# Kernel tuning notes

Measured on AMD Instinct MI355X. Metric: run time of the kernel, lower is better.

Reference implementation:

```python
import jax, jax.numpy as jnp
import numpy as np

TEMPERATURE = 0.1

def setup_inputs() -> dict:
    key = jax.random.key(0)
    ks = jax.random.split(key, 6)
    B, K, D, H, N = 256, 32, 128, 256, 16
    z = jax.random.normal(ks[0], (B, K, D), dtype=jnp.float32)
    # edge MLP params: Linear(2D->H), GELU, Linear(H->D)
    W1 = jax.random.normal(ks[1], (2 * D, H), dtype=jnp.float32) * (1.0 / np.sqrt(2 * D))
    b1 = jnp.zeros((H,), dtype=jnp.float32)
    W2 = jax.random.normal(ks[2], (H, D), dtype=jnp.float32) * (1.0 / np.sqrt(H))
    b2 = jnp.zeros((D,), dtype=jnp.float32)
    codebook = jax.random.normal(ks[3], (N, D), dtype=jnp.float32) * 0.02
    return {"z": z, "W1": W1, "b1": b1, "W2": W2, "b2": b2, "codebook": codebook}

def reference(z, W1, b1, W2, b2, codebook):
    # z: (B,K,D). Edge MLP on concat([z_i, z_j]) == split-weight GEMMs,
    # avoiding materializing the (B,K,K,2D) concat tensor.
    D = z.shape[-1]
    h_i = jnp.einsum('bkd,dh->bkh', z, W1[:D])   # contribution of z_i
    h_j = jnp.einsum('bkd,dh->bkh', z, W1[D:])   # contribution of z_j
    h = h_i[:, :, None, :] + h_j[:, None, :, :] + b1       # (B,K,K,H)
    h = jax.nn.gelu(h, approximate=False)                    # torch nn.GELU default = exact erf
    e_ij = jnp.einsum('bijh,hd->bijd', h, W2) + b2           # (B,K,K,D)
    logits = jnp.einsum('bijd,nd->bijn', e_ij, codebook) / TEMPERATURE  # (B,K,K,N)
    alpha_ij = jax.nn.softmax(logits, axis=-1)
    m_ij = jnp.einsum('bijn,nd->bijd', alpha_ij, codebook)   # (B,K,K,D)
    return (m_ij, alpha_ij, e_ij, logits)
```

## Files before the change

kernel.cpp:

```cpp
#include <hip/hip_runtime.h>
#include <hip/hip_bf16.h>
#include <math.h>

#define BB 256
#define KK 32
#define DD 128
#define HH 256
#define NN 16
#define O0 ((size_t)0)
#define O1 ((size_t)33554432)
#define O2 ((size_t)37748736)
#define O3 ((size_t)71303168)

typedef float f32x4 __attribute__((ext_vector_type(4)));
typedef short s16x8 __attribute__((ext_vector_type(8)));

static __device__ __forceinline__ short f2bf(float x) {
  __hip_bfloat16 h = __float2bfloat16(x);
  return *reinterpret_cast<short*>(&h);
}
static __device__ __forceinline__ float bf2f(short s) {
  __hip_bfloat16 h;
  *reinterpret_cast<short*>(&h) = s;
  return __bfloat162float(h);
}

static __device__ __forceinline__ float gelu_exact(float x) {
  float ax = fabsf(x) * 0.70710678118654752f;
  float t = __builtin_amdgcn_rcpf(fmaf(0.3275911f, ax, 1.0f));
  float p = fmaf(1.061405429f, t, -1.453152027f);
  p = fmaf(p, t, 1.421413741f);
  p = fmaf(p, t, -0.284496736f);
  p = fmaf(p, t, 0.254829592f);
  p *= t;
  float e = __expf(-ax * ax);
  float er = fmaf(-p, e, 1.0f);
  er = copysignf(er, x);
  return 0.5f * x * (1.0f + er);
}

__global__ __launch_bounds__(256) void prep_kernel(
    const float* __restrict__ z, const float* __restrict__ W1,
    const float* __restrict__ W2, const float* __restrict__ cb,
    short* __restrict__ zb, short* __restrict__ W1th, short* __restrict__ W1tl,
    short* __restrict__ Wh, short* __restrict__ Wl,
    short* __restrict__ cbh, short* __restrict__ cbl) {
  const int idx = blockIdx.x * 256 + threadIdx.x;
  zb[idx] = f2bf(z[idx]);
  if (idx < 512 * 128) {
    int c = idx >> 7, k = idx & 127;
    float w = (c < 256) ? W1[(size_t)k * 256 + c]
                        : W1[(size_t)(128 + k) * 256 + (c - 256)];
    short h = f2bf(w);
    W1th[idx] = h;
    W1tl[idx] = f2bf(w - bf2f(h));
  }
  if (idx < 128 * 256) {
    int c = idx >> 8, k = idx & 255;
    float w = W2[(size_t)k * 128 + c];
    short h = f2bf(w);
    Wh[idx] = h;
    Wl[idx] = f2bf(w - bf2f(h));
  }
  if (idx < 2048) {
    float v = cb[idx];
    short h = f2bf(v);
    cbh[idx] = h;
    cbl[idx] = f2bf(v - bf2f(h));
  }
}

__global__ __launch_bounds__(256) void hproj_mfma(
    const short* __restrict__ zb, const short* __restrict__ W1th,
    const short* __restrict__ W1tl, float* __restrict__ H) {
  const int tid = threadIdx.x;
  const int lane = tid & 63;
  const int wv = tid >> 6;
  const int l4 = lane >> 4, l15 = lane & 15;
  const int row0 = blockIdx.x * 32;
  const int col0 = blockIdx.y * 128 + wv * 32;

  f32x4 acc[2][2];
#pragma unroll
  for (int mt = 0; mt < 2; ++mt)
#pragma unroll
    for (int nt = 0; nt < 2; ++nt)
      acc[mt][nt] = (f32x4){0.f, 0.f, 0.f, 0.f};

#pragma unroll
  for (int ks = 0; ks < 4; ++ks) {
    const int kof = ks * 32 + l4 * 8;
    s16x8 a0 = *(const s16x8*)(zb + (size_t)(row0 + l15) * 128 + kof);
    s16x8 a1 = *(const s16x8*)(zb + (size_t)(row0 + 16 + l15) * 128 + kof);
    s16x8 bh0 = *(const s16x8*)(W1th + (size_t)(col0 + l15) * 128 + kof);
    s16x8 bh1 = *(const s16x8*)(W1th + (size_t)(col0 + 16 + l15) * 128 + kof);
    s16x8 bl0 = *(const s16x8*)(W1tl + (size_t)(col0 + l15) * 128 + kof);
    s16x8 bl1 = *(const s16x8*)(W1tl + (size_t)(col0 + 16 + l15) * 128 + kof);
    acc[0][0] = __builtin_amdgcn_mfma_f32_16x16x32_bf16(a0, bh0, acc[0][0], 0, 0, 0);
    acc[0][0] = __builtin_amdgcn_mfma_f32_16x16x32_bf16(a0, bl0, acc[0][0], 0, 0, 0);
    acc[0][1] = __builtin_amdgcn_mfma_f32_16x16x32_bf16(a0, bh1, acc[0][1], 0, 0, 0);
    acc[0][1] = __builtin_amdgcn_mfma_f32_16x16x32_bf16(a0, bl1, acc[0][1], 0, 0, 0);
    acc[1][0] = __builtin_amdgcn_mfma_f32_16x16x32_bf16(a1, bh0, acc[1][0], 0, 0, 0);
    acc[1][0] = __builtin_amdgcn_mfma_f32_16x16x32_bf16(a1, bl0, acc[1][0], 0, 0, 0);
    acc[1][1] = __builtin_amdgcn_mfma_f32_16x16x32_bf16(a1, bh1, acc[1][1], 0, 0, 0);
    acc[1][1] = __builtin_amdgcn_mfma_f32_16x16x32_bf16(a1, bl1, acc[1][1], 0, 0, 0);
  }

#pragma unroll
  for (int mt = 0; mt < 2; ++mt)
#pragma unroll
    for (int nt = 0; nt < 2; ++nt)
#pragma unroll
      for (int r = 0; r < 4; ++r)
        H[(size_t)(row0 + mt * 16 + l4 * 4 + r) * 512 + col0 + nt * 16 + l15] =
            acc[mt][nt][r];
}

__global__ __launch_bounds__(256, 4) void pair_kernel(
    const float* __restrict__ Hcat, const float* __restrict__ b1,
    const short* __restrict__ Wh, const short* __restrict__ Wl,
    const float* __restrict__ b2, const float* __restrict__ cb,
    const short* __restrict__ cbh, const short* __restrict__ cbl,
    float* __restrict__ out) {
  __shared__ short sAh[32 * 256];
  __shared__ union {
    short Al[32 * 256];
    struct { short Eh[32 * 128]; short El[32 * 128]; } e;
  } u;
  __shared__ float sAlp[32][16];

  const int tid = threadIdx.x;
  const int blk = blockIdx.x;
  const int b = blk >> 5;

  {
    const int k0 = (tid & 127) * 2;
    const int pb = (tid >> 7) * 16;
    const float2 hiv = *(const float2*)(Hcat + (size_t)blk * 512 + k0);
    const float2 b1v = *(const float2*)(b1 + k0);
    const float hx = hiv.x + b1v.x;
    const float hy = hiv.y + b1v.y;
    const float* hjp = Hcat + ((size_t)b * KK + pb) * 512 + 256 + k0;
    unsigned* aH = (unsigned*)sAh;
    unsigned* aL = (unsigned*)u.Al;
    const int cw = tid & 127;
#pragma unroll 4
    for (int p = 0; p < 16; ++p) {
      const int row = pb + p;
      float2 hj = *(const float2*)(hjp + (size_t)p * 512);
      float g0 = gelu_exact(hx + hj.x);
      float g1 = gelu_exact(hy + hj.y);
      short h0 = f2bf(g0), h1 = f2bf(g1);
      short l0 = f2bf(g0 - bf2f(h0)), l1 = f2bf(g1 - bf2f(h1));
      const int wi = row * 128 + ((cw ^ ((row & 7) << 2)));
      aH[wi] = (unsigned)(unsigned short)h0 | ((unsigned)(unsigned short)h1 << 16);
      aL[wi] = (unsigned)(unsigned short)l0 | ((unsigned)(unsigned short)l1 << 16);
    }
  }
  __syncthreads();

  const int lane = tid & 63;
  const int wv = tid >> 6;
  const int nb = wv * 32;
  const int l4 = lane >> 4;
  const int l15 = lane & 15;

  f32x4 acc[2][2];
#pragma unroll
  for (int mt = 0; mt < 2; ++mt)
#pragma unroll
    for (int nt = 0; nt < 2; ++nt)
      acc[mt][nt] = (f32x4){0.f, 0.f, 0.f, 0.f};

  const int sw = (l15 & 7) << 4;
  const char* pAh = (const char*)sAh;
  const char* pAl = (const char*)u.Al;
  const size_t gB0 = (size_t)(nb + l15) * 256 + l4 * 8;

#pragma unroll
  for (int ks = 0; ks < 8; ++ks) {
    const int cbyte = ks * 64 + l4 * 16;
    const int o0 = l15 * 512 + (cbyte ^ sw);
    const int o1 = (16 + l15) * 512 + (cbyte ^ sw);
    s16x8 ah0 = *(const s16x8*)(pAh + o0);
    s16x8 ah1 = *(const s16x8*)(pAh + o1);
    s16x8 al0 = *(const s16x8*)(pAl + o0);
    s16x8 al1 = *(const s16x8*)(pAl + o1);
    const size_t g0 = gB0 + ks * 32;
    const size_t g1 = g0 + 16 * 256;
    s16x8 bh0 = *(const s16x8*)(Wh + g0);
    s16x8 bh1 = *(const s16x8*)(Wh + g1);
    s16x8 bl0 = *(const s16x8*)(Wl + g0);
    s16x8 bl1 = *(const s16x8*)(Wl + g1);

    acc[0][0] = __builtin_amdgcn_mfma_f32_16x16x32_bf16(ah0, bh0, acc[0][0], 0, 0, 0);
    acc[0][0] = __builtin_amdgcn_mfma_f32_16x16x32_bf16(al0, bh0, acc[0][0], 0, 0, 0);
    acc[0][0] = __builtin_amdgcn_mfma_f32_16x16x32_bf16(ah0, bl0, acc[0][0], 0, 0, 0);
    acc[0][1] = __builtin_amdgcn_mfma_f32_16x16x32_bf16(ah0, bh1, acc[0][1], 0, 0, 0);
    acc[0][1] = __builtin_amdgcn_mfma_f32_16x16x32_bf16(al0, bh1, acc[0][1], 0, 0, 0);
    acc[0][1] = __builtin_amdgcn_mfma_f32_16x16x32_bf16(ah0, bl1, acc[0][1], 0, 0, 0);
    acc[1][0] = __builtin_amdgcn_mfma_f32_16x16x32_bf16(ah1, bh0, acc[1][0], 0, 0, 0);
    acc[1][0] = __builtin_amdgcn_mfma_f32_16x16x32_bf16(al1, bh0, acc[1][0], 0, 0, 0);
    acc[1][0] = __builtin_amdgcn_mfma_f32_16x16x32_bf16(ah1, bl0, acc[1][0], 0, 0, 0);
    acc[1][1] = __builtin_amdgcn_mfma_f32_16x16x32_bf16(ah1, bh1, acc[1][1], 0, 0, 0);
    acc[1][1] = __builtin_amdgcn_mfma_f32_16x16x32_bf16(al1, bh1, acc[1][1], 0, 0, 0);
    acc[1][1] = __builtin_amdgcn_mfma_f32_16x16x32_bf16(ah1, bl1, acc[1][1], 0, 0, 0);
  }

  __syncthreads();

  {
    const float b2v0 = b2[nb + l15];
    const float b2v1 = b2[nb + 16 + l15];
    float* eg = out + O2 + (size_t)blk * (KK * DD);
    char* pEh = (char*)u.e.Eh;
    char* pEl = (char*)u.e.El;
#pragma unroll
    for (int mt = 0; mt < 2; ++mt) {
#pragma unroll
      for (int r = 0; r < 4; ++r) {
        const int row = mt * 16 + l4 * 4 + r;
        const int rsw = (row & 7) << 4;
        const float e0 = acc[mt][0][r] + b2v0;
        const float e1 = acc[mt][1][r] + b2v1;
        eg[row * 128 + nb + l15] = e0;
        eg[row * 128 + nb + 16 + l15] = e1;
        short h0 = f2bf(e0), h1 = f2bf(e1);
        short lo0 = f2bf(e0 - bf2f(h0)), lo1 = f2bf(e1 - bf2f(h1));
        const int i0 = row * 256 + (((nb + l15) * 2) ^ rsw);
        const int i1 = row * 256 + (((nb + 16 + l15) * 2) ^ rsw);
        *(short*)(pEh + i0) = h0;
        *(short*)(pEh + i1) = h1;
        *(short*)(pEl + i0) = lo0;
        *(short*)(pEl + i1) = lo1;
      }
    }
  }
  __syncthreads();

  if (wv < 2) {
    const int mrow = wv * 16;
    f32x4 lacc = (f32x4){0.f, 0.f, 0.f, 0.f};
    const char* pEh = (const char*)u.e.Eh;
    const char* pEl = (const char*)u.e.El;
    const int rowa = mrow + l15;
    const int rsw = (rowa & 7) << 4;
#pragma unroll
    for (int ks = 0; ks < 4; ++ks) {
      const int cbyte = ks * 64 + l4 * 16;
      const int o = rowa * 256 + (cbyte ^ rsw);
      s16x8 eh = *(const s16x8*)(pEh + o);
      s16x8 el = *(const s16x8*)(pEl + o);
      const size_t g = (size_t)l15 * 128 + ks * 32 + l4 * 8;
      s16x8 ch = *(const s16x8*)(cbh + g);
      s16x8 cl = *(const s16x8*)(cbl + g);
      lacc = __builtin_amdgcn_mfma_f32_16x16x32_bf16(eh, ch, lacc, 0, 0, 0);
      lacc = __builtin_amdgcn_mfma_f32_16x16x32_bf16(el, ch, lacc, 0, 0, 0);
      lacc = __builtin_amdgcn_mfma_f32_16x16x32_bf16(eh, cl, lacc, 0, 0, 0);
    }
    float* lg_out = out + O3 + (size_t)blk * (KK * NN);
    float* ag_out = out + O1 + (size_t)blk * (KK * NN);
#pragma unroll
    for (int r = 0; r < 4; ++r) {
      const int row = mrow + l4 * 4 + r;
      float lg = lacc[r] * 10.0f;
      float mx = lg;
#pragma unroll
      for (int m = 1; m < 16; m <<= 1) mx = fmaxf(mx, __shfl_xor(mx, m));
      float p = __expf(lg - mx);
      float s = p;
#pragma unroll
      for (int m = 1; m < 16; m <<= 1) s += __shfl_xor(s, m);
      float a = p / s;
      lg_out[row * 16 + l15] = lg;
      ag_out[row * 16 + l15] = a;
      sAlp[row][l15] = a;
    }
  }
  __syncthreads();

  {
    const int pg = tid >> 5;
    const int cg = tid & 31;
    const float4* cb4 = (const float4*)cb;
    float4 mac0 = make_float4(0.f, 0.f, 0.f, 0.f);
    float4 mac1 = mac0, mac2 = mac0, mac3 = mac0;
#pragma unroll
    for (int n = 0; n < 16; ++n) {
      float4 cv = cb4[n * 32 + cg];
      float a0 = sAlp[pg * 4 + 0][n];
      float a1 = sAlp[pg * 4 + 1][n];
      float a2 = sAlp[pg * 4 + 2][n];
      float a3 = sAlp[pg * 4 + 3][n];
      mac0.x += a0 * cv.x; mac0.y += a0 * cv.y; mac0.z += a0 * cv.z; mac0.w += a0 * cv.w;
      mac1.x += a1 * cv.x; mac1.y += a1 * cv.y; mac1.z += a1 * cv.z; mac1.w += a1 * cv.w;
      mac2.x += a2 * cv.x; mac2.y += a2 * cv.y; mac2.z += a2 * cv.z; mac2.w += a2 * cv.w;
      mac3.x += a3 * cv.x; mac3.y += a3 * cv.y; mac3.z += a3 * cv.z; mac3.w += a3 * cv.w;
    }
    float* mg = out + O0 + (size_t)blk * (KK * DD);
    *(float4*)(mg + (size_t)(pg * 4 + 0) * 128 + cg * 4) = mac0;
    *(float4*)(mg + (size_t)(pg * 4 + 1) * 128 + cg * 4) = mac1;
    *(float4*)(mg + (size_t)(pg * 4 + 2) * 128 + cg * 4) = mac2;
    *(float4*)(mg + (size_t)(pg * 4 + 3) * 128 + cg * 4) = mac3;
  }
}

extern "C" void kernel_launch(void* const* d_in, const int* in_sizes, int n_in,
                              void* d_out, int out_size, void* d_ws, size_t ws_size,
                              hipStream_t stream) {
  const float* z  = (const float*)d_in[0];
  const float* W1 = (const float*)d_in[1];
  const float* b1 = (const float*)d_in[2];
  const float* W2 = (const float*)d_in[3];
  const float* b2 = (const float*)d_in[4];
  const float* cb = (const float*)d_in[5];
  float* out = (float*)d_out;

  float* Hcat = (float*)d_ws;
  short* zb   = (short*)(Hcat + (size_t)8192 * 512);
  short* W1th = zb + (size_t)1048576;
  short* W1tl = W1th + (size_t)65536;
  short* Wh   = W1tl + (size_t)65536;
  short* Wl   = Wh + (size_t)32768;
  short* cbh  = Wl + (size_t)32768;
  short* cbl  = cbh + (size_t)2048;

  prep_kernel<<<4096, 256, 0, stream>>>(z, W1, W2, cb, zb, W1th, W1tl, Wh, Wl, cbh, cbl);
  hproj_mfma<<<dim3(256, 4), 256, 0, stream>>>(zb, W1th, W1tl, Hcat);
  pair_kernel<<<BB * KK, 256, 0, stream>>>(Hcat, b1, Wh, Wl, b2, cb, cbh, cbl, out);
}
```

Baseline: 209.3 us.

## Split pair kernel into half-row blocks and compute alpha·codebook via bf16 MFMA

Each pair_kernel block now handles 16 j-pairs instead of 32, doubling the grid and halving shared memory. Launch bounds are raised to 8 blocks per SIMD for higher occupancy. The final alpha·codebook product is moved from a scalar FMA loop to one bf16 MFMA per 16-column tile, using a transposed, zero-padded codebook built in the prep kernel. Alpha and codebook are rounded to single bf16 with no hi/lo split, which costs some accuracy in m_ij. The W2 B-fragments are now reloaded from global by twice as many blocks.

```diff
diff --git a/kernel.cpp b/kernel.cpp
--- a/kernel.cpp
+++ b/kernel.cpp
@@ -44,7 +44,7 @@
     const float* __restrict__ W2, const float* __restrict__ cb,
     short* __restrict__ zb, short* __restrict__ W1th, short* __restrict__ W1tl,
     short* __restrict__ Wh, short* __restrict__ Wl,
-    short* __restrict__ cbh, short* __restrict__ cbl) {
+    short* __restrict__ cbh, short* __restrict__ cbl, short* __restrict__ cbT) {
   const int idx = blockIdx.x * 256 + threadIdx.x;
   zb[idx] = f2bf(z[idx]);
   if (idx < 512 * 128) {
@@ -67,6 +67,10 @@
     short h = f2bf(v);
     cbh[idx] = h;
     cbl[idx] = f2bf(v - bf2f(h));
+  }
+  if (idx < 128 * 32) {
+    int c = idx >> 5, n = idx & 31;
+    cbT[idx] = (n < 16) ? f2bf(cb[(size_t)n * 128 + c]) : (short)0;
   }
 }
 
@@ -116,36 +120,40 @@
             acc[mt][nt][r];
 }
 
-__global__ __launch_bounds__(256, 4) void pair_kernel(
+__global__ __launch_bounds__(256, 8) void pair_kernel(
     const float* __restrict__ Hcat, const float* __restrict__ b1,
     const short* __restrict__ Wh, const short* __restrict__ Wl,
-    const float* __restrict__ b2, const float* __restrict__ cb,
-    const short* __restrict__ cbh, const short* __restrict__ cbl,
+    const float* __restrict__ b2, const short* __restrict__ cbh,
+    const short* __restrict__ cbl, const short* __restrict__ cbT,
     float* __restrict__ out) {
-  __shared__ short sAh[32 * 256];
+  __shared__ short sAh[16 * 256];
   __shared__ union {
-    short Al[32 * 256];
-    struct { short Eh[32 * 128]; short El[32 * 128]; } e;
+    short Al[16 * 256];
+    struct { short Eh[16 * 128]; short El[16 * 128]; } e;
   } u;
-  __shared__ float sAlp[32][16];
+  __shared__ short sAlp[16 * 32];
 
   const int tid = threadIdx.x;
   const int blk = blockIdx.x;
-  const int b = blk >> 5;
+  const int bi = blk >> 1;
+  const int b = blk >> 6;
+  const int j0 = (blk & 1) * 16;
+
+  ((unsigned*)sAlp)[tid] = 0u;
 
   {
     const int k0 = (tid & 127) * 2;
-    const int pb = (tid >> 7) * 16;
-    const float2 hiv = *(const float2*)(Hcat + (size_t)blk * 512 + k0);
+    const int pb = (tid >> 7) * 8;
+    const float2 hiv = *(const float2*)(Hcat + (size_t)bi * 512 + k0);
     const float2 b1v = *(const float2*)(b1 + k0);
     const float hx = hiv.x + b1v.x;
     const float hy = hiv.y + b1v.y;
-    const float* hjp = Hcat + ((size_t)b * KK + pb) * 512 + 256 + k0;
+    const float* hjp = Hcat + ((size_t)b * KK + j0 + pb) * 512 + 256 + k0;
     unsigned* aH = (unsigned*)sAh;
     unsigned* aL = (unsigned*)u.Al;
     const int cw = tid & 127;
 #pragma unroll 4
-    for (int p = 0; p < 16; ++p) {
+    for (int p = 0; p < 8; ++p) {
       const int row = pb + p;
       float2 hj = *(const float2*)(hjp + (size_t)p * 512);
       float g0 = gelu_exact(hx + hj.x);
@@ -165,12 +173,8 @@
   const int l4 = lane >> 4;
   const int l15 = lane & 15;
 
-  f32x4 acc[2][2];
-#pragma unroll
-  for (int mt = 0; mt < 2; ++mt)
-#pragma unroll
-    for (int nt = 0; nt < 2; ++nt)
-      acc[mt][nt] = (f32x4){0.f, 0.f, 0.f, 0.f};
+  f32x4 acc0 = (f32x4){0.f, 0.f, 0.f, 0.f};
+  f32x4 acc1 = (f32x4){0.f, 0.f, 0.f, 0.f};
 
   const int sw = (l15 & 7) << 4;
   const char* pAh = (const char*)sAh;
@@ -181,11 +185,8 @@
   for (int ks = 0; ks < 8; ++ks) {
     const int cbyte = ks * 64 + l4 * 16;
     const int o0 = l15 * 512 + (cbyte ^ sw);
-    const int o1 = (16 + l15) * 512 + (cbyte ^ sw);
-    s16x8 ah0 = *(const s16x8*)(pAh + o0);
-    s16x8 ah1 = *(const s16x8*)(pAh + o1);
-    s16x8 al0 = *(const s16x8*)(pAl + o0);
-    s16x8 al1 = *(const s16x8*)(pAl + o1);
+    s16x8 ah = *(const s16x8*)(pAh + o0);
+    s16x8 al = *(const s16x8*)(pAl + o0);
     const size_t g0 = gB0 + ks * 32;
     const size_t g1 = g0 + 16 * 256;
     s16x8 bh0 = *(const s16x8*)(Wh + g0);
@@ -193,18 +194,12 @@
     s16x8 bl0 = *(const s16x8*)(Wl + g0);
     s16x8 bl1 = *(const s16x8*)(Wl + g1);
 
-    acc[0][0] = __builtin_amdgcn_mfma_f32_16x16x32_bf16(ah0, bh0, acc[0][0], 0, 0, 0);
-    acc[0][0] = __builtin_amdgcn_mfma_f32_16x16x32_bf16(al0, bh0, acc[0][0], 0, 0, 0);
-    acc[0][0] = __builtin_amdgcn_mfma_f32_16x16x32_bf16(ah0, bl0, acc[0][0], 0, 0, 0);
-    acc[0][1] = __builtin_amdgcn_mfma_f32_16x16x32_bf16(ah0, bh1, acc[0][1], 0, 0, 0);
-    acc[0][1] = __builtin_amdgcn_mfma_f32_16x16x32_bf16(al0, bh1, acc[0][1], 0, 0, 0);
-    acc[0][1] = __builtin_amdgcn_mfma_f32_16x16x32_bf16(ah0, bl1, acc[0][1], 0, 0, 0);
-    acc[1][0] = __builtin_amdgcn_mfma_f32_16x16x32_bf16(ah1, bh0, acc[1][0], 0, 0, 0);
-    acc[1][0] = __builtin_amdgcn_mfma_f32_16x16x32_bf16(al1, bh0, acc[1][0], 0, 0, 0);
-    acc[1][0] = __builtin_amdgcn_mfma_f32_16x16x32_bf16(ah1, bl0, acc[1][0], 0, 0, 0);
-    acc[1][1] = __builtin_amdgcn_mfma_f32_16x16x32_bf16(ah1, bh1, acc[1][1], 0, 0, 0);
-    acc[1][1] = __builtin_amdgcn_mfma_f32_16x16x32_bf16(al1, bh1, acc[1][1], 0, 0, 0);
-    acc[1][1] = __builtin_amdgcn_mfma_f32_16x16x32_bf16(ah1, bl1, acc[1][1], 0, 0, 0);
+    acc0 = __builtin_amdgcn_mfma_f32_16x16x32_bf16(ah, bh0, acc0, 0, 0, 0);
+    acc0 = __builtin_amdgcn_mfma_f32_16x16x32_bf16(al, bh0, acc0, 0, 0, 0);
+    acc0 = __builtin_amdgcn_mfma_f32_16x16x32_bf16(ah, bl0, acc0, 0, 0, 0);
+    acc1 = __builtin_amdgcn_mfma_f32_16x16x32_bf16(ah, bh1, acc1, 0, 0, 0);
+    acc1 = __builtin_amdgcn_mfma_f32_16x16x32_bf16(al, bh1, acc1, 0, 0, 0);
+    acc1 = __builtin_amdgcn_mfma_f32_16x16x32_bf16(ah, bl1, acc1, 0, 0, 0);
   }
 
   __syncthreads();
@@ -212,43 +207,38 @@
   {
     const float b2v0 = b2[nb + l15];
     const float b2v1 = b2[nb + 16 + l15];
-    float* eg = out + O2 + (size_t)blk * (KK * DD);
+    float* eg = out + O2 + ((size_t)bi * KK + j0) * DD;
     char* pEh = (char*)u.e.Eh;
     char* pEl = (char*)u.e.El;
 #pragma unroll
-    for (int mt = 0; mt < 2; ++mt) {
-#pragma unroll
-      for (int r = 0; r < 4; ++r) {
-        const int row = mt * 16 + l4 * 4 + r;
-        const int rsw = (row & 7) << 4;
-        const float e0 = acc[mt][0][r] + b2v0;
-        const float e1 = acc[mt][1][r] + b2v1;
-        eg[row * 128 + nb + l15] = e0;
-        eg[row * 128 + nb + 16 + l15] = e1;
-        short h0 = f2bf(e0), h1 = f2bf(e1);
-        short lo0 = f2bf(e0 - bf2f(h0)), lo1 = f2bf(e1 - bf2f(h1));
-        const int i0 = row * 256 + (((nb + l15) * 2) ^ rsw);
-        const int i1 = row * 256 + (((nb + 16 + l15) * 2) ^ rsw);
-        *(short*)(pEh + i0) = h0;
-        *(short*)(pEh + i1) = h1;
-        *(short*)(pEl + i0) = lo0;
-        *(short*)(pEl + i1) = lo1;
-      }
+    for (int r = 0; r < 4; ++r) {
+      const int row = l4 * 4 + r;
+      const int rsw = (row & 7) << 4;
+      const float e0 = acc0[r] + b2v0;
+      const float e1 = acc1[r] + b2v1;
+      eg[row * 128 + nb + l15] = e0;
+      eg[row * 128 + nb + 16 + l15] = e1;
+      short h0 = f2bf(e0), h1 = f2bf(e1);
+      short lo0 = f2bf(e0 - bf2f(h0)), lo1 = f2bf(e1 - bf2f(h1));
+      const int i0 = row * 256 + (((nb + l15) * 2) ^ rsw);
+      const int i1 = row * 256 + (((nb + 16 + l15) * 2) ^ rsw);
+      *(short*)(pEh + i0) = h0;
+      *(short*)(pEh + i1) = h1;
+      *(short*)(pEl + i0) = lo0;
+      *(short*)(pEl + i1) = lo1;
     }
   }
   __syncthreads();
 
-  if (wv < 2) {
-    const int mrow = wv * 16;
+  if (wv == 0) {
     f32x4 lacc = (f32x4){0.f, 0.f, 0.f, 0.f};
     const char* pEh = (const char*)u.e.Eh;
     const char* pEl = (const char*)u.e.El;
-    const int rowa = mrow + l15;
-    const int rsw = (rowa & 7) << 4;
+    const int rsw = (l15 & 7) << 4;
 #pragma unroll
     for (int ks = 0; ks < 4; ++ks) {
       const int cbyte = ks * 64 + l4 * 16;
-      const int o = rowa * 256 + (cbyte ^ rsw);
+      const int o = l15 * 256 + (cbyte ^ rsw);
       s16x8 eh = *(const s16x8*)(pEh + o);
       s16x8 el = *(const s16x8*)(pEl + o);
       const size_t g = (size_t)l15 * 128 + ks * 32 + l4 * 8;
@@ -258,11 +248,11 @@
       lacc = __builtin_amdgcn_mfma_f32_16x16x32_bf16(el, ch, lacc, 0, 0, 0);
       lacc = __builtin_amdgcn_mfma_f32_16x16x32_bf16(eh, cl, lacc, 0, 0, 0);
     }
-    float* lg_out = out + O3 + (size_t)blk * (KK * NN);
-    float* ag_out = out + O1 + (size_t)blk * (KK * NN);
+    float* lg_out = out + O3 + ((size_t)bi * KK + j0) * NN;
+    float* ag_out = out + O1 + ((size_t)bi * KK + j0) * NN;
 #pragma unroll
     for (int r = 0; r < 4; ++r) {
-      const int row = mrow + l4 * 4 + r;
+      const int row = l4 * 4 + r;
       float lg = lacc[r] * 10.0f;
       float mx = lg;
 #pragma unroll
@@ -274,34 +264,24 @@
       float a = p / s;
       lg_out[row * 16 + l15] = lg;
       ag_out[row * 16 + l15] = a;
-      sAlp[row][l15] = a;
+      sAlp[row * 32 + l15] = f2bf(a);
     }
   }
   __syncthreads();
 
   {
-    const int pg = tid >> 5;
-    const int cg = tid & 31;
-    const float4* cb4 = (const float4*)cb;
-    float4 mac0 = make_float4(0.f, 0.f, 0.f, 0.f);
-    float4 mac1 = mac0, mac2 = mac0, mac3 = mac0;
-#pragma unroll
-    for (int n = 0; n < 16; ++n) {
-      float4 cv = cb4[n * 32 + cg];
-      float a0 = sAlp[pg * 4 + 0][n];
-      float a1 = sAlp[pg * 4 + 1][n];
-      float a2 = sAlp[pg * 4 + 2][n];
-      float a3 = sAlp[pg * 4 + 3][n];
-      mac0.x += a0 * cv.x; mac0.y += a0 * cv.y; mac0.z += a0 * cv.z; mac0.w += a0 * cv.w;
-      mac1.x += a1 * cv.x; mac1.y += a1 * cv.y; mac1.z += a1 * cv.z; mac1.w += a1 * cv.w;
-      mac2.x += a2 * cv.x; mac2.y += a2 * cv.y; mac2.z += a2 * cv.z; mac2.w += a2 * cv.w;
-      mac3.x += a3 * cv.x; mac3.y += a3 * cv.y; mac3.z += a3 * cv.z; mac3.w += a3 * cv.w;
-    }
-    float* mg = out + O0 + (size_t)blk * (KK * DD);
-    *(float4*)(mg + (size_t)(pg * 4 + 0) * 128 + cg * 4) = mac0;
-    *(float4*)(mg + (size_t)(pg * 4 + 1) * 128 + cg * 4) = mac1;
-    *(float4*)(mg + (size_t)(pg * 4 + 2) * 128 + cg * 4) = mac2;
-    *(float4*)(mg + (size_t)(pg * 4 + 3) * 128 + cg * 4) = mac3;
+    s16x8 af = *(const s16x8*)(sAlp + l15 * 32 + l4 * 8);
+    float* mg = out + O0 + ((size_t)bi * KK + j0) * DD;
+#pragma unroll
+    for (int nt = 0; nt < 2; ++nt) {
+      const int c = nb + nt * 16 + l15;
+      s16x8 bf = *(const s16x8*)(cbT + (size_t)c * 32 + l4 * 8);
+      f32x4 mac = (f32x4){0.f, 0.f, 0.f, 0.f};
+      mac = __builtin_amdgcn_mfma_f32_16x16x32_bf16(af, bf, mac, 0, 0, 0);
+#pragma unroll
+      for (int r = 0; r < 4; ++r)
+        mg[(l4 * 4 + r) * 128 + c] = mac[r];
+    }
   }
 }
 
@@ -324,8 +304,11 @@
   short* Wl   = Wh + (size_t)32768;
   short* cbh  = Wl + (size_t)32768;
   short* cbl  = cbh + (size_t)2048;
-
-  prep_kernel<<<4096, 256, 0, stream>>>(z, W1, W2, cb, zb, W1th, W1tl, Wh, Wl, cbh, cbl);
+  short* cbT  = cbl + (size_t)2048;
+
+  prep_kernel<<<4096, 256, 0, stream>>>(z, W1, W2, cb, zb, W1th, W1tl, Wh, Wl,
+                                        cbh, cbl, cbT);
   hproj_mfma<<<dim3(256, 4), 256, 0, stream>>>(zb, W1th, W1tl, Hcat);
-  pair_kernel<<<BB * KK, 256, 0, stream>>>(Hcat, b1, Wh, Wl, b2, cb, cbh, cbl, out);
-}
+  pair_kernel<<<BB * KK * 2, 256, 0, stream>>>(Hcat, b1, Wh, Wl, b2, cbh, cbl,
+                                               cbT, out);
+}
```

After: 304.2 us. 1.45x slower.

## Use MFMA for alpha-codebook product, packed bf16 converts, fold b1 into projection

Applied to the files above, without the earlier changes.

The final m_ij = alpha·codebook product is moved from scalar FMAs with global float4 codebook loads onto a single bf16 MFMA per tile. It uses a zero-padded transposed bf16 codebook and alpha stored as bf16 in shared memory. The hi/lo bf16 splits now use the packed v_cvt_pk_bf16_f32 instruction, and b1 is added once in the projection kernel instead of per pair. Rounding alpha and the codebook to single bf16 with no lo term lowers the precision of m_ij.

```diff
diff --git a/kernel.cpp b/kernel.cpp
--- a/kernel.cpp
+++ b/kernel.cpp
@@ -23,6 +23,11 @@
   __hip_bfloat16 h;
   *reinterpret_cast<short*>(&h) = s;
   return __bfloat162float(h);
+}
+static __device__ __forceinline__ unsigned cvt_pk_bf16(float a, float b) {
+  unsigned r;
+  asm volatile("v_cvt_pk_bf16_f32 %0, %1, %2" : "=v"(r) : "v"(a), "v"(b));
+  return r;
 }
 
 static __device__ __forceinline__ float gelu_exact(float x) {
@@ -44,7 +49,7 @@
     const float* __restrict__ W2, const float* __restrict__ cb,
     short* __restrict__ zb, short* __restrict__ W1th, short* __restrict__ W1tl,
     short* __restrict__ Wh, short* __restrict__ Wl,
-    short* __restrict__ cbh, short* __restrict__ cbl) {
+    short* __restrict__ cbh, short* __restrict__ cbl, short* __restrict__ cbT) {
   const int idx = blockIdx.x * 256 + threadIdx.x;
   zb[idx] = f2bf(z[idx]);
   if (idx < 512 * 128) {
@@ -68,11 +73,16 @@
     cbh[idx] = h;
     cbl[idx] = f2bf(v - bf2f(h));
   }
+  if (idx < 128 * 32) {
+    int c = idx >> 5, n = idx & 31;
+    cbT[idx] = (n < 16) ? f2bf(cb[(size_t)n * 128 + c]) : (short)0;
+  }
 }
 
 __global__ __launch_bounds__(256) void hproj_mfma(
     const short* __restrict__ zb, const short* __restrict__ W1th,
-    const short* __restrict__ W1tl, float* __restrict__ H) {
+    const short* __restrict__ W1tl, const float* __restrict__ b1,
+    float* __restrict__ H) {
   const int tid = threadIdx.x;
   const int lane = tid & 63;
   const int wv = tid >> 6;
@@ -107,39 +117,43 @@
   }
 
 #pragma unroll
-  for (int mt = 0; mt < 2; ++mt)
-#pragma unroll
-    for (int nt = 0; nt < 2; ++nt)
+  for (int nt = 0; nt < 2; ++nt) {
+    const int col = col0 + nt * 16 + l15;
+    const float bias = (col0 < 256) ? b1[col] : 0.f;
+#pragma unroll
+    for (int mt = 0; mt < 2; ++mt)
 #pragma unroll
       for (int r = 0; r < 4; ++r)
-        H[(size_t)(row0 + mt * 16 + l4 * 4 + r) * 512 + col0 + nt * 16 + l15] =
-            acc[mt][nt][r];
+        H[(size_t)(row0 + mt * 16 + l4 * 4 + r) * 512 + col] =
+            acc[mt][nt][r] + bias;
+  }
 }
 
 __global__ __launch_bounds__(256, 4) void pair_kernel(
-    const float* __restrict__ Hcat, const float* __restrict__ b1,
-    const short* __restrict__ Wh, const short* __restrict__ Wl,
-    const float* __restrict__ b2, const float* __restrict__ cb,
+    const float* __restrict__ Hcat, const short* __restrict__ Wh,
+    const short* __restrict__ Wl, const float* __restrict__ b2,
     const short* __restrict__ cbh, const short* __restrict__ cbl,
-    float* __restrict__ out) {
+    const short* __restrict__ cbT, float* __restrict__ out) {
   __shared__ short sAh[32 * 256];
   __shared__ union {
     short Al[32 * 256];
     struct { short Eh[32 * 128]; short El[32 * 128]; } e;
   } u;
-  __shared__ float sAlp[32][16];
+  __shared__ short sAlp[32 * 32];
 
   const int tid = threadIdx.x;
   const int blk = blockIdx.x;
   const int b = blk >> 5;
+
+  ((unsigned*)sAlp)[tid] = 0u;
+  ((unsigned*)sAlp)[tid + 256] = 0u;
 
   {
     const int k0 = (tid & 127) * 2;
     const int pb = (tid >> 7) * 16;
     const float2 hiv = *(const float2*)(Hcat + (size_t)blk * 512 + k0);
-    const float2 b1v = *(const float2*)(b1 + k0);
-    const float hx = hiv.x + b1v.x;
-    const float hy = hiv.y + b1v.y;
+    const float hx = hiv.x;
+    const float hy = hiv.y;
     const float* hjp = Hcat + ((size_t)b * KK + pb) * 512 + 256 + k0;
     unsigned* aH = (unsigned*)sAh;
     unsigned* aL = (unsigned*)u.Al;
@@ -150,11 +164,13 @@
       float2 hj = *(const float2*)(hjp + (size_t)p * 512);
       float g0 = gelu_exact(hx + hj.x);
       float g1 = gelu_exact(hy + hj.y);
-      short h0 = f2bf(g0), h1 = f2bf(g1);
-      short l0 = f2bf(g0 - bf2f(h0)), l1 = f2bf(g1 - bf2f(h1));
+      unsigned h01 = cvt_pk_bf16(g0, g1);
+      float h0f = __uint_as_float(h01 << 16);
+      float h1f = __uint_as_float(h01 & 0xFFFF0000u);
+      unsigned l01 = cvt_pk_bf16(g0 - h0f, g1 - h1f);
       const int wi = row * 128 + ((cw ^ ((row & 7) << 2)));
-      aH[wi] = (unsigned)(unsigned short)h0 | ((unsigned)(unsigned short)h1 << 16);
-      aL[wi] = (unsigned)(unsigned short)l0 | ((unsigned)(unsigned short)l1 << 16);
+      aH[wi] = h01;
+      aL[wi] = l01;
     }
   }
   __syncthreads();
@@ -225,14 +241,16 @@
         const float e1 = acc[mt][1][r] + b2v1;
         eg[row * 128 + nb + l15] = e0;
         eg[row * 128 + nb + 16 + l15] = e1;
-        short h0 = f2bf(e0), h1 = f2bf(e1);
-        short lo0 = f2bf(e0 - bf2f(h0)), lo1 = f2bf(e1 - bf2f(h1));
+        unsigned hp = cvt_pk_bf16(e0, e1);
+        float h0f = __uint_as_float(hp << 16);
+        float h1f = __uint_as_float(hp & 0xFFFF0000u);
+        unsigned lp = cvt_pk_bf16(e0 - h0f, e1 - h1f);
         const int i0 = row * 256 + (((nb + l15) * 2) ^ rsw);
         const int i1 = row * 256 + (((nb + 16 + l15) * 2) ^ rsw);
-        *(short*)(pEh + i0) = h0;
-        *(short*)(pEh + i1) = h1;
-        *(short*)(pEl + i0) = lo0;
-        *(short*)(pEl + i1) = lo1;
+        *(short*)(pEh + i0) = (short)(hp & 0xFFFFu);
+        *(short*)(pEh + i1) = (short)(hp >> 16);
+        *(short*)(pEl + i0) = (short)(lp & 0xFFFFu);
+        *(short*)(pEl + i1) = (short)(lp >> 16);
       }
     }
   }
@@ -274,34 +292,27 @@
       float a = p / s;
       lg_out[row * 16 + l15] = lg;
       ag_out[row * 16 + l15] = a;
-      sAlp[row][l15] = a;
+      sAlp[row * 32 + l15] = f2bf(a);
     }
   }
   __syncthreads();
 
   {
-    const int pg = tid >> 5;
-    const int cg = tid & 31;
-    const float4* cb4 = (const float4*)cb;
-    float4 mac0 = make_float4(0.f, 0.f, 0.f, 0.f);
-    float4 mac1 = mac0, mac2 = mac0, mac3 = mac0;
-#pragma unroll
-    for (int n = 0; n < 16; ++n) {
-      float4 cv = cb4[n * 32 + cg];
-      float a0 = sAlp[pg * 4 + 0][n];
-      float a1 = sAlp[pg * 4 + 1][n];
-      float a2 = sAlp[pg * 4 + 2][n];
-      float a3 = sAlp[pg * 4 + 3][n];
-      mac0.x += a0 * cv.x; mac0.y += a0 * cv.y; mac0.z += a0 * cv.z; mac0.w += a0 * cv.w;
-      mac1.x += a1 * cv.x; mac1.y += a1 * cv.y; mac1.z += a1 * cv.z; mac1.w += a1 * cv.w;
-      mac2.x += a2 * cv.x; mac2.y += a2 * cv.y; mac2.z += a2 * cv.z; mac2.w += a2 * cv.w;
-      mac3.x += a3 * cv.x; mac3.y += a3 * cv.y; mac3.z += a3 * cv.z; mac3.w += a3 * cv.w;
-    }
     float* mg = out + O0 + (size_t)blk * (KK * DD);
-    *(float4*)(mg + (size_t)(pg * 4 + 0) * 128 + cg * 4) = mac0;
-    *(float4*)(mg + (size_t)(pg * 4 + 1) * 128 + cg * 4) = mac1;
-    *(float4*)(mg + (size_t)(pg * 4 + 2) * 128 + cg * 4) = mac2;
-    *(float4*)(mg + (size_t)(pg * 4 + 3) * 128 + cg * 4) = mac3;
+#pragma unroll
+    for (int rg = 0; rg < 2; ++rg) {
+      s16x8 af = *(const s16x8*)(sAlp + (rg * 16 + l15) * 32 + l4 * 8);
+#pragma unroll
+      for (int nt = 0; nt < 2; ++nt) {
+        const int c = nb + nt * 16 + l15;
+        s16x8 bf = *(const s16x8*)(cbT + (size_t)c * 32 + l4 * 8);
+        f32x4 mac = (f32x4){0.f, 0.f, 0.f, 0.f};
+        mac = __builtin_amdgcn_mfma_f32_16x16x32_bf16(af, bf, mac, 0, 0, 0);
+#pragma unroll
+        for (int r = 0; r < 4; ++r)
+          mg[(rg * 16 + l4 * 4 + r) * 128 + c] = mac[r];
+      }
+    }
   }
 }
 
@@ -324,8 +335,10 @@
   short* Wl   = Wh + (size_t)32768;
   short* cbh  = Wl + (size_t)32768;
   short* cbl  = cbh + (size_t)2048;
-
-  prep_kernel<<<4096, 256, 0, stream>>>(z, W1, W2, cb, zb, W1th, W1tl, Wh, Wl, cbh, cbl);
-  hproj_mfma<<<dim3(256, 4), 256, 0, stream>>>(zb, W1th, W1tl, Hcat);
-  pair_kernel<<<BB * KK, 256, 0, stream>>>(Hcat, b1, Wh, Wl, b2, cb, cbh, cbl, out);
-}
+  short* cbT  = cbl + (size_t)2048;
+
+  prep_kernel<<<4096, 256, 0, stream>>>(z, W1, W2, cb, zb, W1th, W1tl, Wh, Wl,
+                                        cbh, cbl, cbT);
+  hproj_mfma<<<dim3(256, 4), 256, 0, stream>>>(zb, W1th, W1tl, b1, Hcat);
+  pair_kernel<<<BB * KK, 256, 0, stream>>>(Hcat, Wh, Wl, b2, cbh, cbl, cbT, out);
+}
```

New measurement: 201.1 us. 3.9% less time.
